# Kernel optimization log

Hardware: AMD Instinct MI355X
Metric: run time of the kernel (lower is better)

## Reference

```python
import jax, jax.numpy as jnp
import numpy as np

OUTPUT_DIM = 1024  # init kwarg output_dim


def _adaptive_avg_pool_last(x, out_dim):
    """Faithful F.adaptive_avg_pool1d over the last axis (static shapes)."""
    in_dim = x.shape[-1]
    if in_dim % out_dim == 0:
        k = in_dim // out_dim
        return x.reshape(x.shape[:-1] + (out_dim, k)).mean(axis=-1)
    # generic case: window i covers [floor(i*In/Out), ceil((i+1)*In/Out))
    idx = np.arange(out_dim)
    starts = (idx * in_dim) // out_dim
    ends = -((-(idx + 1) * in_dim) // out_dim)
    W = np.zeros((in_dim, out_dim), dtype=np.float32)
    for i in range(out_dim):
        W[starts[i]:ends[i], i] = 1.0 / (ends[i] - starts[i])
    return x @ jnp.asarray(W)


def _per_layer_gram(feat, output_dim):
    N, C, ph, pw = feat.shape
    P = ph * pw
    c_red = min(C, 64)
    f = feat.reshape(N, C, P).transpose(0, 2, 1)        # [N, P, C]
    f = _adaptive_avg_pool_last(f, c_red)               # [N, P, Cr] channel reduction
    fr = f.transpose(0, 2, 1)                           # [N, Cr, P]
    gram = jnp.einsum('ncp,ndp->ncd', fr, fr) / P       # [N, Cr, Cr] per-patch Gram
    return _adaptive_avg_pool_last(gram.reshape(N, c_red * c_red), output_dim)  # [N, output_dim]


def setup_inputs() -> dict:
    key = jax.random.key(0)
    k0, k1 = jax.random.split(key)
    feat0 = jax.random.normal(k0, (6272, 512, 3, 3), dtype=jnp.float32)
    feat1 = jax.random.normal(k1, (6272, 1024, 3, 3), dtype=jnp.float32)
    return {"feat0": feat0, "feat1": feat1}


def reference(feat0, feat1):
    # stack over layers -> [N, L=2, output_dim]
    return jnp.stack(
        [_per_layer_gram(feat0, OUTPUT_DIM), _per_layer_gram(feat1, OUTPUT_DIM)],
        axis=1,
    )
```

## Files before the change

### kernel.cpp

```cpp
#include <hip/hip_runtime.h>


#define N_SAMPLES 6272

typedef const __attribute__((address_space(1))) void* gas_ptr;
typedef __attribute__((address_space(3))) void* las_ptr;

__device__ __forceinline__ void load16_to_lds(const void* g, void* l) {
    __builtin_amdgcn_global_load_lds((gas_ptr)g, (las_ptr)l, 16, 0, 0);
}

template <int CH>
__global__ __launch_bounds__(256) void patchgram_layer(
    const float* __restrict__ src, float* __restrict__ out)
{
    constexpr int NF   = CH * 9;
    constexpr int NV4  = NF / 4;
    constexpr int GSH  = (CH == 1024) ? 2 : 1;
    constexpr int NRED = 64 << GSH;
    constexpr int K    = CH / 64;
    constexpr float SCALE = 1.0f / (36.0f * (float)(K * K));

    __shared__ float4 tile[NV4];
    __shared__ float4 fr4[64 * 3];
    __shared__ float4 B4[16 * 3];

    const int n = blockIdx.x;
    const int t = threadIdx.x;

    const float4* __restrict__ g = (const float4*)(src + (size_t)n * NF);
    for (int i = t; i < NV4; i += 256)
        load16_to_lds(&g[i], &tile[i]);
    __syncthreads();

    if (t < NRED) {
        const float4* __restrict__ tp = &tile[t * 9];
        float acc[9];
#pragma unroll
        for (int p = 0; p < 9; ++p) acc[p] = 0.f;
#pragma unroll
        for (int j = 0; j < 9; ++j) {
            const float4 v = tp[j];
            acc[(4 * j + 0) % 9] += v.x;
            acc[(4 * j + 1) % 9] += v.y;
            acc[(4 * j + 2) % 9] += v.z;
            acc[(4 * j + 3) % 9] += v.w;
        }
#pragma unroll
        for (int p = 0; p < 9; ++p) acc[p] += __shfl_xor(acc[p], 1);
        if (GSH == 2) {
#pragma unroll
            for (int p = 0; p < 9; ++p) acc[p] += __shfl_xor(acc[p], 2);
        }
        if ((t & ((1 << GSH) - 1)) == 0) {
            const int row = t >> GSH;
            fr4[row * 3 + 0] = make_float4(acc[0], acc[1], acc[2], acc[3]);
            fr4[row * 3 + 1] = make_float4(acc[4], acc[5], acc[6], acc[7]);
            fr4[row * 3 + 2] = make_float4(acc[8], 0.f, 0.f, 0.f);
        }
    }
    __syncthreads();

    if (t < 144) {
        const int dg = t / 9;
        const int p  = t - dg * 9;
        const float* fr = (const float*)fr4;
        ((float*)B4)[dg * 12 + p] =
            fr[(4 * dg + 0) * 12 + p] + fr[(4 * dg + 1) * 12 + p] +
            fr[(4 * dg + 2) * 12 + p] + fr[(4 * dg + 3) * 12 + p];
    }
    __syncthreads();

    const int c   = t >> 2;
    const int dgq = t & 3;
    const float4 a0 = fr4[c * 3 + 0];
    const float4 a1 = fr4[c * 3 + 1];
    const float4 a2 = fr4[c * 3 + 2];

    float4 o4;
    float* op = (float*)&o4;
#pragma unroll
    for (int j = 0; j < 4; ++j) {
        const int d = dgq * 4 + j;
        const float4 b0 = B4[d * 3 + 0];
        const float4 b1 = B4[d * 3 + 1];
        const float4 b2 = B4[d * 3 + 2];
        float s = a0.x * b0.x + a0.y * b0.y + a0.z * b0.z + a0.w * b0.w
                + a1.x * b1.x + a1.y * b1.y + a1.z * b1.z + a1.w * b1.w
                + a2.x * b2.x;
        op[j] = s * SCALE;
    }
    float4* o = (float4*)(out + (size_t)n * 2048 + c * 16 + dgq * 4);
    *o = o4;
}

extern "C" void kernel_launch(void* const* d_in, const int* in_sizes, int n_in,
                              void* d_out, int out_size, void* d_ws, size_t ws_size,
                              hipStream_t stream) {
    const float* f0 = (const float*)d_in[0];
    const float* f1 = (const float*)d_in[1];
    float* out = (float*)d_out;
    patchgram_layer<512><<<N_SAMPLES, 256, 0, stream>>>(f0, out);
    patchgram_layer<1024><<<N_SAMPLES, 256, 0, stream>>>(f1, out + 1024);
}
```

Before: 388.0 us.

## Fuse both layer kernels into one launch with halved LDS tile for layer1

Merges the two per-layer launches into one grid that interleaves layer0 and layer1 blocks. The 1024-channel layer now streams its 36 KB sample through an 18 KB LDS tile in two halves, so every block uses the same smaller shared-memory footprint and more blocks can be resident (launch_bounds min 6 blocks). This aims to raise occupancy and overlap the traffic of both layers in a memory-bound kernel. The cost is an extra load-sync round for layer1 blocks and a runtime branch on the layer.

New measurement: 391.9 us. About the same (+1.0%).

```diff
diff --git a/kernel.cpp b/kernel.cpp
--- a/kernel.cpp
+++ b/kernel.cpp
@@ -10,31 +10,16 @@
     __builtin_amdgcn_global_load_lds((gas_ptr)g, (las_ptr)l, 16, 0, 0);
 }
 
-template <int CH>
-__global__ __launch_bounds__(256) void patchgram_layer(
-    const float* __restrict__ src, float* __restrict__ out)
-{
-    constexpr int NF   = CH * 9;
-    constexpr int NV4  = NF / 4;
-    constexpr int GSH  = (CH == 1024) ? 2 : 1;
-    constexpr int NRED = 64 << GSH;
-    constexpr int K    = CH / 64;
-    constexpr float SCALE = 1.0f / (36.0f * (float)(K * K));
+struct Smem {
+    float4 tile[1152];
+    float4 fr4[64 * 3];
+    float4 B4[16 * 3];
+};
 
-    __shared__ float4 tile[NV4];
-    __shared__ float4 fr4[64 * 3];
-    __shared__ float4 B4[16 * 3];
-
-    const int n = blockIdx.x;
-    const int t = threadIdx.x;
-
-    const float4* __restrict__ g = (const float4*)(src + (size_t)n * NF);
-    for (int i = t; i < NV4; i += 256)
-        load16_to_lds(&g[i], &tile[i]);
-    __syncthreads();
-
-    if (t < NRED) {
-        const float4* __restrict__ tp = &tile[t * 9];
+template <int GSH>
+__device__ __forceinline__ void reduce_tile(Smem& sm, int t, int row_base) {
+    if (t < 128) {
+        const float4* __restrict__ tp = &sm.tile[t * 9];
         float acc[9];
 #pragma unroll
         for (int p = 0; p < 9; ++p) acc[p] = 0.f;
@@ -53,19 +38,47 @@
             for (int p = 0; p < 9; ++p) acc[p] += __shfl_xor(acc[p], 2);
         }
         if ((t & ((1 << GSH) - 1)) == 0) {
-            const int row = t >> GSH;
-            fr4[row * 3 + 0] = make_float4(acc[0], acc[1], acc[2], acc[3]);
-            fr4[row * 3 + 1] = make_float4(acc[4], acc[5], acc[6], acc[7]);
-            fr4[row * 3 + 2] = make_float4(acc[8], 0.f, 0.f, 0.f);
+            const int row = row_base + (t >> GSH);
+            sm.fr4[row * 3 + 0] = make_float4(acc[0], acc[1], acc[2], acc[3]);
+            sm.fr4[row * 3 + 1] = make_float4(acc[4], acc[5], acc[6], acc[7]);
+            sm.fr4[row * 3 + 2] = make_float4(acc[8], 0.f, 0.f, 0.f);
         }
     }
-    __syncthreads();
+}
+
+__global__ __launch_bounds__(256, 6) void patchgram_kernel(
+    const float* __restrict__ f0, const float* __restrict__ f1,
+    float* __restrict__ out)
+{
+    __shared__ Smem sm;
+    const int b     = blockIdx.x;
+    const int t     = threadIdx.x;
+    const int layer = b & 1;
+    const int n     = b >> 1;
+
+    if (!layer) {
+        const float4* __restrict__ g = (const float4*)(f0 + (size_t)n * 4608);
+        for (int i = t; i < 1152; i += 256) load16_to_lds(&g[i], &sm.tile[i]);
+        __syncthreads();
+        reduce_tile<1>(sm, t, 0);
+        __syncthreads();
+    } else {
+        const float4* __restrict__ g = (const float4*)(f1 + (size_t)n * 9216);
+#pragma unroll
+        for (int h = 0; h < 2; ++h) {
+            for (int i = t; i < 1152; i += 256)
+                load16_to_lds(&g[h * 1152 + i], &sm.tile[i]);
+            __syncthreads();
+            reduce_tile<2>(sm, t, h * 32);
+            __syncthreads();
+        }
+    }
 
     if (t < 144) {
         const int dg = t / 9;
         const int p  = t - dg * 9;
-        const float* fr = (const float*)fr4;
-        ((float*)B4)[dg * 12 + p] =
+        const float* fr = (const float*)sm.fr4;
+        ((float*)sm.B4)[dg * 12 + p] =
             fr[(4 * dg + 0) * 12 + p] + fr[(4 * dg + 1) * 12 + p] +
             fr[(4 * dg + 2) * 12 + p] + fr[(4 * dg + 3) * 12 + p];
     }
@@ -73,24 +86,25 @@
 
     const int c   = t >> 2;
     const int dgq = t & 3;
-    const float4 a0 = fr4[c * 3 + 0];
-    const float4 a1 = fr4[c * 3 + 1];
-    const float4 a2 = fr4[c * 3 + 2];
+    const float4 a0 = sm.fr4[c * 3 + 0];
+    const float4 a1 = sm.fr4[c * 3 + 1];
+    const float4 a2 = sm.fr4[c * 3 + 2];
+    const float scale = layer ? (1.0f / (36.0f * 256.0f))
+                              : (1.0f / (36.0f * 64.0f));
 
     float4 o4;
     float* op = (float*)&o4;
 #pragma unroll
     for (int j = 0; j < 4; ++j) {
         const int d = dgq * 4 + j;
-        const float4 b0 = B4[d * 3 + 0];
-        const float4 b1 = B4[d * 3 + 1];
-        const float4 b2 = B4[d * 3 + 2];
-        float s = a0.x * b0.x + a0.y * b0.y + a0.z * b0.z + a0.w * b0.w
-                + a1.x * b1.x + a1.y * b1.y + a1.z * b1.z + a1.w * b1.w
-                + a2.x * b2.x;
-        op[j] = s * SCALE;
+        const float4 b0 = sm.B4[d * 3 + 0];
+        const float4 b1 = sm.B4[d * 3 + 1];
+        const float4 b2 = sm.B4[d * 3 + 2];
+        op[j] = (a0.x * b0.x + a0.y * b0.y + a0.z * b0.z + a0.w * b0.w
+               + a1.x * b1.x + a1.y * b1.y + a1.z * b1.z + a1.w * b1.w
+               + a2.x * b2.x) * scale;
     }
-    float4* o = (float4*)(out + (size_t)n * 2048 + c * 16 + dgq * 4);
+    float4* o = (float4*)(out + (size_t)n * 2048 + layer * 1024 + c * 16 + dgq * 4);
     *o = o4;
 }
 
@@ -100,6 +114,5 @@
     const float* f0 = (const float*)d_in[0];
     const float* f1 = (const float*)d_in[1];
     float* out = (float*)d_out;
-    patchgram_layer<512><<<N_SAMPLES, 256, 0, stream>>>(f0, out);
-    patchgram_layer<1024><<<N_SAMPLES, 256, 0, stream>>>(f1, out + 1024);
+    patchgram_kernel<<<N_SAMPLES * 2, 256, 0, stream>>>(f0, f1, out);
 }
```
